# Kernel optimization log

Hardware: AMD Instinct MI355X
Metric: run time of the kernel (lower is better)

## Reference

```python
import jax, jax.numpy as jnp
import numpy as np

EPS = 1e-5


def _bn_relu(h, gamma, beta):
    # BatchNorm1d in training mode: stats over all but the last (channel) dim
    m = h.reshape(-1, h.shape[-1])
    mu = jnp.mean(m, axis=0)
    var = jnp.var(m, axis=0)
    return jax.nn.relu((h - mu) * jax.lax.rsqrt(var + EPS) * gamma + beta)


def setup_inputs() -> dict:
    key = jax.random.key(0)
    ks = jax.random.split(key, 16)
    B, N, D, OUT = 64, 64, 64, 128
    T = 2 * D          # object_tuple_size = 128
    HG, HF = 256, 128  # hidden_dim_g, hidden_dim_f

    def lin(k, i, o):
        return (jax.random.normal(k, (i, o), jnp.float32) / np.sqrt(i).astype(np.float32),
                jnp.zeros((o,), jnp.float32))

    inp = {"x": jax.random.normal(ks[0], (B, N, D), jnp.float32)}
    # G: depth-3 Linear-BN-ReLU, dims T -> HG -> HG -> T
    for i, (a, b) in enumerate([(T, HG), (HG, HG), (HG, T)]):
        W, bb = lin(ks[1 + i], a, b)
        inp[f"gW{i}"] = W
        inp[f"gb{i}"] = bb
        inp[f"gg{i}"] = jnp.ones((b,), jnp.float32)
        inp[f"gB{i}"] = jnp.zeros((b,), jnp.float32)
    # F: depth-2 Linear-BN-ReLU, dims T -> HF -> T, then Linear(T, OUT)
    for i, (a, b) in enumerate([(T, HF), (HF, T)]):
        W, bb = lin(ks[5 + i], a, b)
        inp[f"fW{i}"] = W
        inp[f"fb{i}"] = bb
        inp[f"fg{i}"] = jnp.ones((b,), jnp.float32)
        inp[f"fB{i}"] = jnp.zeros((b,), jnp.float32)
    inp["foW"], inp["fob"] = lin(ks[8], T, OUT)
    return inp


def reference(x, gW0, gb0, gg0, gB0, gW1, gb1, gg1, gB1, gW2, gb2, gg2, gB2,
              fW0, fb0, fg0, fB0, fW1, fb1, fg1, fB1, foW, fob):
    B, N, D = x.shape
    # GroupObjectsIntoPairs: all ordered pairs -> (B, N*N, 2D)
    xi = jnp.broadcast_to(x[:, :, None, :], (B, N, N, D))
    xj = jnp.broadcast_to(x[:, None, :, :], (B, N, N, D))
    h = jnp.concatenate([xi, xj], axis=-1).reshape(B, N * N, 2 * D)
    # G: per-pair MLP
    for W, b, g, be in ((gW0, gb0, gg0, gB0), (gW1, gb1, gg1, gB1), (gW2, gb2, gg2, gB2)):
        h = _bn_relu(h @ W + b, g, be)
    # sum over pair dimension (no layer norm)
    s = h.sum(axis=1)  # (B, 2D)
    # F: MLP + final linear
    for W, b, g, be in ((fW0, fb0, fg0, fB0), (fW1, fb1, fg1, fB1)):
        s = _bn_relu(s @ W + b, g, be)
    return s @ foW + fob  # (B, OUT)
```

## Files before the change

### kernel.cpp

```cpp
#include <hip/hip_runtime.h>


typedef _Float16 half8 __attribute__((ext_vector_type(8)));
typedef _Float16 half4_t __attribute__((ext_vector_type(4)));
typedef float float4_t __attribute__((ext_vector_type(4)));

static constexpr float kEps = 1e-5f;
static constexpr float kM = 262144.f;

static constexpr size_t OFF_U   = 0;
static constexpr size_t OFF_V   = OFF_U  + (size_t)4096*256*4;
static constexpr size_t OFF_UP  = OFF_V  + (size_t)4096*256*4;
static constexpr size_t OFF_VP  = OFF_UP + (size_t)4096*256*2;
static constexpr size_t OFF_W1T = OFF_VP + (size_t)4096*256*2;
static constexpr size_t OFF_W2T = OFF_W1T + (size_t)256*256*2;
static constexpr size_t OFF_Z1  = OFF_W2T + (size_t)128*256*2;
static constexpr size_t OFF_ST0 = OFF_Z1 + (size_t)262144*256*2;
static constexpr size_t OFF_C0S = OFF_ST0 + (size_t)64*4*256*4;
static constexpr size_t OFF_C0T = OFF_C0S + 1024;
static constexpr size_t OFF_C1S = OFF_C0T + 1024;
static constexpr size_t OFF_C1T = OFF_C1S + 1024;
static constexpr size_t OFF_C2S = OFF_C1T + 1024;
static constexpr size_t OFF_C2T = OFF_C2S + 512;
static constexpr size_t OFF_ST1 = OFF_C2T + 512;
static constexpr size_t OFF_ST2 = OFF_ST1 + (size_t)32*512*4;
static constexpr size_t OFF_SB  = OFF_ST2 + (size_t)32*256*4;
static constexpr size_t OFF_FST0 = OFF_SB + (size_t)64*128*4;
static constexpr size_t OFF_FST1 = OFF_FST0 + 1024;
static constexpr size_t ZERO_BYTES = (size_t)32*512*4 + (size_t)32*256*4
                                   + (size_t)64*128*4 + 2048;
static constexpr size_t OFF_FZ0  = OFF_FST1 + 1024;
static constexpr size_t OFF_FZ1  = OFF_FZ0 + (size_t)64*128*4;
static constexpr size_t OFF_CF0S = OFF_FZ1 + (size_t)64*128*4;
static constexpr size_t OFF_CF0T = OFF_CF0S + 512;
static constexpr size_t OFF_CF1S = OFF_CF0T + 512;
static constexpr size_t OFF_CF1T = OFF_CF1S + 512;
static constexpr size_t OFF_C1H  = OFF_CF1T + 512;
static constexpr size_t OFF_Z2   = OFF_C1H + 1024;
static constexpr size_t WS_REQUIRED = OFF_Z2 + (size_t)262144*128*2;

static __device__ inline half8 relu8(half8 s) {
#pragma unroll
  for (int e = 0; e < 8; ++e) s[e] = s[e] > (_Float16)0 ? s[e] : (_Float16)0;
  return s;
}

__global__ __launch_bounds__(256) void k_wt(const float* __restrict__ gW1,
                                            const float* __restrict__ gW2,
                                            _Float16* __restrict__ W1T,
                                            _Float16* __restrict__ W2T) {
  int idx = blockIdx.x * 256 + threadIdx.x;
  if (idx < 65536) {
    int n = idx >> 8, k = idx & 255;
    W1T[idx] = (_Float16)gW1[k * 256 + n];
  } else if (idx < 98304) {
    int j = idx - 65536;
    int n = j >> 8, k = j & 255;
    W2T[j] = (_Float16)gW2[k * 128 + n];
  }
}

__global__ __launch_bounds__(256) void k_prep(const float* __restrict__ x,
                                              const float* __restrict__ gW0,
                                              float* __restrict__ U,
                                              float* __restrict__ V) {
  __shared__ __align__(16) float sX[32 * 64];
  int t = threadIdx.x;
  int p0 = blockIdx.x * 32;
  int by = blockIdx.y;
  int hsel = by >> 1;
  int cbase = (by & 1) * 128;
#pragma unroll
  for (int it = 0; it < 2; ++it) {
    int f4 = (it * 256 + t) * 4;
    *(float4_t*)(sX + f4) = *(const float4_t*)(x + (size_t)p0 * 64 + f4);
  }
  __syncthreads();
  int r = t >> 3, cg = (t & 7) * 16;
  const float* Wb = gW0 + (size_t)(hsel * 64) * 256 + cbase + cg;
  float acc[16];
#pragma unroll
  for (int j = 0; j < 16; ++j) acc[j] = 0.f;
  for (int k = 0; k < 64; ++k) {
    float xv = sX[r * 64 + k];
    const float4_t* wr = (const float4_t*)(Wb + (size_t)k * 256);
    float4_t w0 = wr[0], w1 = wr[1], w2 = wr[2], w3 = wr[3];
#pragma unroll
    for (int j = 0; j < 4; ++j) {
      acc[j]      += xv * w0[j];
      acc[4 + j]  += xv * w1[j];
      acc[8 + j]  += xv * w2[j];
      acc[12 + j] += xv * w3[j];
    }
  }
  float* outp = (hsel ? V : U) + (size_t)(p0 + r) * 256 + cbase + cg;
#pragma unroll
  for (int q = 0; q < 4; ++q) {
    float4_t o = {acc[q * 4], acc[q * 4 + 1], acc[q * 4 + 2], acc[q * 4 + 3]};
    *(float4_t*)(outp + q * 4) = o;
  }
}

__global__ __launch_bounds__(256) void k_stats0(const float* __restrict__ U,
                                                const float* __restrict__ V,
                                                float* __restrict__ st0) {
  int b = blockIdx.x, c = threadIdx.x;
  float su = 0, su2 = 0, sv = 0, sv2 = 0;
  for (int i = 0; i < 64; ++i) {
    float u = U[(size_t)(b * 64 + i) * 256 + c];
    float v = V[(size_t)(b * 64 + i) * 256 + c];
    su += u; su2 += u * u; sv += v; sv2 += v * v;
  }
  st0[(b * 4 + 0) * 256 + c] = su;
  st0[(b * 4 + 1) * 256 + c] = su2;
  st0[(b * 4 + 2) * 256 + c] = sv;
  st0[(b * 4 + 3) * 256 + c] = sv2;
}

__global__ __launch_bounds__(256) void k_bn0(const float* __restrict__ st0,
                                             const float* __restrict__ gb0,
                                             const float* __restrict__ gg0,
                                             const float* __restrict__ gB0,
                                             float* __restrict__ c0s,
                                             float* __restrict__ c0t) {
  int c = threadIdx.x;
  float su = 0, su2 = 0, sv = 0, sv2 = 0, cross = 0;
  for (int b = 0; b < 64; ++b) {
    float a  = st0[(b * 4 + 0) * 256 + c];
    float a2 = st0[(b * 4 + 1) * 256 + c];
    float v  = st0[(b * 4 + 2) * 256 + c];
    float v2 = st0[(b * 4 + 3) * 256 + c];
    su += a; su2 += a2; sv += v; sv2 += v2; cross += a * v;
  }
  float b0 = gb0[c];
  float sumz  = 64.f * (su + sv) + kM * b0;
  float sumzz = 64.f * (su2 + sv2) + 2.f * cross + 2.f * b0 * 64.f * (su + sv) + kM * b0 * b0;
  float mu = sumz / kM;
  float var = sumzz / kM - mu * mu;
  float sc = gg0[c] * rsqrtf(var + kEps);
  c0s[c] = sc;
  c0t[c] = gB0[c] + sc * (b0 - mu);
}

__global__ __launch_bounds__(256) void k_uv(const float* __restrict__ U,
                                            const float* __restrict__ V,
                                            const float* __restrict__ c0s,
                                            const float* __restrict__ c0t,
                                            _Float16* __restrict__ Up,
                                            _Float16* __restrict__ Vp) {
  int idx = blockIdx.x * 256 + threadIdx.x;
  int e4 = idx * 4;
  int c4 = e4 & 255;
  float4_t u = *(const float4_t*)(U + e4);
  float4_t v = *(const float4_t*)(V + e4);
  float4_t s = *(const float4_t*)(c0s + c4);
  float4_t tt = *(const float4_t*)(c0t + c4);
  half4_t hu, hv;
#pragma unroll
  for (int e = 0; e < 4; ++e) {
    hu[e] = (_Float16)(u[e] * s[e] + tt[e]);
    hv[e] = (_Float16)(v[e] * s[e]);
  }
  *(half4_t*)(Up + e4) = hu;
  *(half4_t*)(Vp + e4) = hv;
}

__global__ __launch_bounds__(256) void k_gemm1(const _Float16* __restrict__ Up,
                                               const _Float16* __restrict__ Vp,
                                               const _Float16* __restrict__ W1T,
                                               const float* __restrict__ gb1,
                                               _Float16* __restrict__ Z1,
                                               float* __restrict__ stats1) {
  __shared__ __align__(16) char smem[128 * 136 * 2];
  _Float16* sU = (_Float16*)smem;
  _Float16* sV = (_Float16*)(smem + 288);
  _Float16* sW = (_Float16*)(smem + 288 + 64 * 72 * 2);
  _Float16* sO = (_Float16*)smem;

  const int t = threadIdx.x;
  const int bx = blockIdx.x;
  const int n0 = blockIdx.y * 128;
  const int b = bx >> 5;
  const int i0 = (bx & 31) * 2;
  const long R0 = (long)bx * 128;

  const int wid = t >> 6, L = t & 63;
  const int wrow = wid >> 1, wcol = wid & 1;
  const int quad = L >> 4, l15 = L & 15;

  float4_t acc[4][4];
#pragma unroll
  for (int mt = 0; mt < 4; ++mt)
#pragma unroll
    for (int nt = 0; nt < 4; ++nt) acc[mt][nt] = (float4_t){0.f, 0.f, 0.f, 0.f};

  for (int kc = 0; kc < 4; ++kc) {
    __syncthreads();
    if (t < 16) {
      int row = t >> 3, c8 = (t & 7) * 8;
      *(half8*)(sU + row * 72 + c8) =
          *(const half8*)(Up + (size_t)(b * 64 + i0 + row) * 256 + kc * 64 + c8);
    }
#pragma unroll
    for (int it = 0; it < 2; ++it) {
      int flat = it * 256 + t;
      int row = flat >> 3, c8 = (flat & 7) * 8;
      *(half8*)(sV + row * 72 + c8) =
          *(const half8*)(Vp + (size_t)(b * 64 + row) * 256 + kc * 64 + c8);
    }
#pragma unroll
    for (int it = 0; it < 4; ++it) {
      int flat = it * 256 + t;
      int row = flat >> 3, c8 = (flat & 7) * 8;
      *(half8*)(sW + row * 72 + c8) =
          *(const half8*)(W1T + (size_t)(n0 + row) * 256 + kc * 64 + c8);
    }
    __syncthreads();
#pragma unroll
    for (int ks = 0; ks < 2; ++ks) {
      const int kk = ks * 32 + quad * 8;
      const half8 u = *(const half8*)(sU + wrow * 72 + kk);
      half8 afr[4];
#pragma unroll
      for (int mt = 0; mt < 4; ++mt) {
        half8 v = *(const half8*)(sV + (mt * 16 + l15) * 72 + kk);
        afr[mt] = relu8(u + v);
      }
      half8 bfr[4];
#pragma unroll
      for (int nt = 0; nt < 4; ++nt)
        bfr[nt] = *(const half8*)(sW + (wcol * 64 + nt * 16 + l15) * 72 + kk);
#pragma unroll
      for (int mt = 0; mt < 4; ++mt)
#pragma unroll
        for (int nt = 0; nt < 4; ++nt)
          acc[mt][nt] = __builtin_amdgcn_mfma_f32_16x16x32_f16(afr[mt], bfr[nt],
                                                               acc[mt][nt], 0, 0, 0);
    }
  }

  __syncthreads();
  const int rep = bx & 31;
#pragma unroll
  for (int nt = 0; nt < 4; ++nt) {
    const int lcol = wcol * 64 + nt * 16 + l15;
    const float b1c = gb1[n0 + lcol];
    float sz = 0.f, szz = 0.f;
#pragma unroll
    for (int mt = 0; mt < 4; ++mt) {
      const int lrow = wrow * 64 + mt * 16 + quad * 4;
#pragma unroll
      for (int r = 0; r < 4; ++r) {
        float z = acc[mt][nt][r] + b1c;
        sO[(lrow + r) * 136 + lcol] = (_Float16)z;
        sz += z;
        szz += z * z;
      }
    }
    sz += __shfl_xor(sz, 16, 64);
    sz += __shfl_xor(sz, 32, 64);
    szz += __shfl_xor(szz, 16, 64);
    szz += __shfl_xor(szz, 32, 64);
    if (quad == 0) {
      atomicAdd(stats1 + rep * 512 + n0 + lcol, sz);
      atomicAdd(stats1 + rep * 512 + 256 + n0 + lcol, szz);
    }
  }
  __syncthreads();
#pragma unroll
  for (int it = 0; it < 8; ++it) {
    int cid = it * 256 + t;
    int row = cid >> 4, ch = (cid & 15) * 8;
    half8 hv = *(const half8*)(sO + row * 136 + ch);
    *(half8*)(Z1 + (size_t)(R0 + row) * 256 + n0 + ch) = hv;
  }
}

__global__ __launch_bounds__(256) void k_bn1(const float* __restrict__ stats1,
                                             const float* __restrict__ gg1,
                                             const float* __restrict__ gB1,
                                             float* __restrict__ c1s,
                                             float* __restrict__ c1t,
                                             _Float16* __restrict__ c1h) {
  int c = threadIdx.x;
  float S = 0.f, S2 = 0.f;
  for (int rp = 0; rp < 32; ++rp) {
    S += stats1[rp * 512 + c];
    S2 += stats1[rp * 512 + 256 + c];
  }
  float mu = S / kM;
  float var = S2 / kM - mu * mu;
  float sc = gg1[c] * rsqrtf(var + kEps);
  float sh = gB1[c] - sc * mu;
  c1s[c] = sc;
  c1t[c] = sh;
  c1h[c] = (_Float16)sc;
  c1h[256 + c] = (_Float16)sh;
}

__global__ __launch_bounds__(256) void k_gemm2(const _Float16* __restrict__ Z1,
                                               const _Float16* __restrict__ W2T,
                                               const _Float16* __restrict__ c1h,
                                               const float* __restrict__ gb2,
                                               _Float16* __restrict__ Z2,
                                               float* __restrict__ stats2) {
  __shared__ __align__(16) char smem[2 * 128 * 72 * 2];
  _Float16* sA = (_Float16*)smem;
  _Float16* sW = (_Float16*)(smem + 128 * 72 * 2);
  _Float16* sO = (_Float16*)smem;
  __shared__ __align__(16) _Float16 sSh[256];
  __shared__ __align__(16) _Float16 sTh[256];
  const int t = threadIdx.x;
  const int bx = blockIdx.x;
  const long R0 = (long)bx * 128;
  sSh[t] = c1h[t];
  sTh[t] = c1h[256 + t];

  const int wid = t >> 6, L = t & 63;
  const int wrow = wid >> 1, wcol = wid & 1;
  const int quad = L >> 4, l15 = L & 15;

  float4_t acc[4][4];
#pragma unroll
  for (int mt = 0; mt < 4; ++mt)
#pragma unroll
    for (int nt = 0; nt < 4; ++nt) acc[mt][nt] = (float4_t){0.f, 0.f, 0.f, 0.f};

  for (int kc = 0; kc < 4; ++kc) {
    __syncthreads();
#pragma unroll
    for (int it = 0; it < 2; ++it) {
      int flat = it * 256 + t;
      int row = flat >> 3, k8 = (flat & 7) * 8;
      int kg = kc * 64 + k8;
      half8 hv = *(const half8*)(Z1 + ((size_t)R0 + row) * 256 + kg);
      half8 hs = *(const half8*)(sSh + kg);
      half8 ht = *(const half8*)(sTh + kg);
      half8 ov = relu8(hv * hs + ht);
      *(half8*)(sA + row * 72 + k8) = ov;
      int row2 = row + 64;
      half8 hv2 = *(const half8*)(Z1 + ((size_t)R0 + row2) * 256 + kg);
      half8 ov2 = relu8(hv2 * hs + ht);
      *(half8*)(sA + row2 * 72 + k8) = ov2;
    }
#pragma unroll
    for (int it = 0; it < 4; ++it) {
      int flat = it * 256 + t;
      int row = flat >> 3, k8 = (flat & 7) * 8;
      *(half8*)(sW + row * 72 + k8) =
          *(const half8*)(W2T + (size_t)row * 256 + kc * 64 + k8);
    }
    __syncthreads();
#pragma unroll
    for (int ks = 0; ks < 2; ++ks) {
      const int kk = ks * 32 + quad * 8;
      half8 afr[4];
#pragma unroll
      for (int mt = 0; mt < 4; ++mt)
        afr[mt] = *(const half8*)(sA + (wrow * 64 + mt * 16 + l15) * 72 + kk);
      half8 bfr[4];
#pragma unroll
      for (int nt = 0; nt < 4; ++nt)
        bfr[nt] = *(const half8*)(sW + (wcol * 64 + nt * 16 + l15) * 72 + kk);
#pragma unroll
      for (int mt = 0; mt < 4; ++mt)
#pragma unroll
        for (int nt = 0; nt < 4; ++nt)
          acc[mt][nt] = __builtin_amdgcn_mfma_f32_16x16x32_f16(afr[mt], bfr[nt],
                                                               acc[mt][nt], 0, 0, 0);
    }
  }

  __syncthreads();
  const int rep = bx & 31;
#pragma unroll
  for (int nt = 0; nt < 4; ++nt) {
    const int lcol = wcol * 64 + nt * 16 + l15;
    const float b2c = gb2[lcol];
    float sz = 0.f, szz = 0.f;
#pragma unroll
    for (int mt = 0; mt < 4; ++mt) {
      const int lrow = wrow * 64 + mt * 16 + quad * 4;
#pragma unroll
      for (int r = 0; r < 4; ++r) {
        float z = acc[mt][nt][r] + b2c;
        sO[(lrow + r) * 136 + lcol] = (_Float16)z;
        sz += z;
        szz += z * z;
      }
    }
    sz += __shfl_xor(sz, 16, 64);
    sz += __shfl_xor(sz, 32, 64);
    szz += __shfl_xor(szz, 16, 64);
    szz += __shfl_xor(szz, 32, 64);
    if (quad == 0) {
      atomicAdd(stats2 + rep * 256 + lcol, sz);
      atomicAdd(stats2 + rep * 256 + 128 + lcol, szz);
    }
  }
  __syncthreads();
#pragma unroll
  for (int it = 0; it < 8; ++it) {
    int cid = it * 256 + t;
    int row = cid >> 4, ch = (cid & 15) * 8;
    half8 hv = *(const half8*)(sO + row * 136 + ch);
    *(half8*)(Z2 + (size_t)(R0 + row) * 128 + ch) = hv;
  }
}

template <int FINAL>
__global__ __launch_bounds__(256) void k_gemm23(const _Float16* __restrict__ Z1,
                                                const _Float16* __restrict__ W2T,
                                                const float* __restrict__ c1s,
                                                const float* __restrict__ c1t,
                                                const float* __restrict__ gb2,
                                                const float* __restrict__ c2s,
                                                const float* __restrict__ c2t,
                                                float* __restrict__ stats2,
                                                float* __restrict__ sbuf) {
  __shared__ __align__(16) _Float16 sA[128 * 72];
  __shared__ __align__(16) _Float16 sW[128 * 72];
  __shared__ __align__(16) float sS[256];
  __shared__ __align__(16) float sT[256];
  const int t = threadIdx.x;
  const int bx = blockIdx.x;
  const long R0 = (long)bx * 128;
  sS[t] = c1s[t];
  sT[t] = c1t[t];

  const int wid = t >> 6, L = t & 63;
  const int wrow = wid >> 1, wcol = wid & 1;
  const int quad = L >> 4, l15 = L & 15;

  float4_t acc[4][4];
#pragma unroll
  for (int mt = 0; mt < 4; ++mt)
#pragma unroll
    for (int nt = 0; nt < 4; ++nt) acc[mt][nt] = (float4_t){0.f, 0.f, 0.f, 0.f};

  for (int kc = 0; kc < 4; ++kc) {
    __syncthreads();
#pragma unroll
    for (int it = 0; it < 4; ++it) {
      int flat = it * 256 + t;
      int row = flat >> 3, k8 = (flat & 7) * 8;
      int kg = kc * 64 + k8;
      half8 hv = *(const half8*)(Z1 + ((size_t)R0 + row) * 256 + kg);
      float4_t s0 = *(const float4_t*)(sS + kg);
      float4_t s1 = *(const float4_t*)(sS + kg + 4);
      float4_t t0 = *(const float4_t*)(sT + kg);
      float4_t t1 = *(const float4_t*)(sT + kg + 4);
      half8 ov;
#pragma unroll
      for (int e = 0; e < 4; ++e) {
        ov[e]     = (_Float16)fmaxf(s0[e] * (float)hv[e] + t0[e], 0.f);
        ov[4 + e] = (_Float16)fmaxf(s1[e] * (float)hv[4 + e] + t1[e], 0.f);
      }
      *(half8*)(sA + row * 72 + k8) = ov;
    }
#pragma unroll
    for (int it = 0; it < 4; ++it) {
      int flat = it * 256 + t;
      int n = flat >> 3, k8 = (flat & 7) * 8;
      *(half8*)(sW + n * 72 + k8) =
          *(const half8*)(W2T + (size_t)n * 256 + kc * 64 + k8);
    }
    __syncthreads();
#pragma unroll
    for (int ks = 0; ks < 2; ++ks) {
      const int kk = ks * 32 + quad * 8;
      half8 afr[4];
#pragma unroll
      for (int mt = 0; mt < 4; ++mt)
        afr[mt] = *(const half8*)(sA + (wrow * 64 + mt * 16 + l15) * 72 + kk);
      half8 bfr[4];
#pragma unroll
      for (int nt = 0; nt < 4; ++nt)
        bfr[nt] = *(const half8*)(sW + (wcol * 64 + nt * 16 + l15) * 72 + kk);
#pragma unroll
      for (int mt = 0; mt < 4; ++mt)
#pragma unroll
        for (int nt = 0; nt < 4; ++nt)
          acc[mt][nt] = __builtin_amdgcn_mfma_f32_16x16x32_f16(afr[mt], bfr[nt],
                                                               acc[mt][nt], 0, 0, 0);
    }
  }

  const int rep = bx & 31;
#pragma unroll
  for (int nt = 0; nt < 4; ++nt) {
    const int col = wcol * 64 + nt * 16 + l15;
    const float b2c = gb2[col];
    if (FINAL) {
      const float s2 = c2s[col], t2 = c2t[col];
      float ps = 0.f;
#pragma unroll
      for (int mt = 0; mt < 4; ++mt)
#pragma unroll
        for (int r = 0; r < 4; ++r)
          ps += fmaxf(s2 * (acc[mt][nt][r] + b2c) + t2, 0.f);
      ps += __shfl_xor(ps, 16, 64);
      ps += __shfl_xor(ps, 32, 64);
      if (quad == 0) atomicAdd(sbuf + (bx >> 5) * 128 + col, ps);
    } else {
      float sz = 0.f, szz = 0.f;
#pragma unroll
      for (int mt = 0; mt < 4; ++mt)
#pragma unroll
        for (int r = 0; r < 4; ++r) {
          float z = acc[mt][nt][r] + b2c;
          sz += z;
          szz += z * z;
        }
      sz += __shfl_xor(sz, 16, 64);
      sz += __shfl_xor(sz, 32, 64);
      szz += __shfl_xor(szz, 16, 64);
      szz += __shfl_xor(szz, 32, 64);
      if (quad == 0) {
        atomicAdd(stats2 + rep * 256 + col, sz);
        atomicAdd(stats2 + rep * 256 + 128 + col, szz);
      }
    }
  }
}

__global__ __launch_bounds__(128) void k_bn2(const float* __restrict__ stats2,
                                             const float* __restrict__ gg2,
                                             const float* __restrict__ gB2,
                                             float* __restrict__ c2s,
                                             float* __restrict__ c2t) {
  int c = threadIdx.x;
  float S = 0.f, S2 = 0.f;
  for (int rp = 0; rp < 32; ++rp) {
    S += stats2[rp * 256 + c];
    S2 += stats2[rp * 256 + 128 + c];
  }
  float mu = S / kM;
  float var = S2 / kM - mu * mu;
  float sc = gg2[c] * rsqrtf(var + kEps);
  c2s[c] = sc;
  c2t[c] = gB2[c] - sc * mu;
}

__global__ __launch_bounds__(256) void k_red(const _Float16* __restrict__ Z2,
                                             const float* __restrict__ c2s,
                                             const float* __restrict__ c2t,
                                             float* __restrict__ sbuf) {
  __shared__ float sR[256 * 8];
  const int t = threadIdx.x;
  const int bx = blockIdx.x;
  const int b = bx >> 5;
  const long row0 = (long)bx * 128;
  const int rr = t >> 4;
  const int c8 = (t & 15) * 8;

  float4_t s0 = *(const float4_t*)(c2s + c8);
  float4_t s1 = *(const float4_t*)(c2s + c8 + 4);
  float4_t t0 = *(const float4_t*)(c2t + c8);
  float4_t t1 = *(const float4_t*)(c2t + c8 + 4);

  float acc[8];
#pragma unroll
  for (int e = 0; e < 8; ++e) acc[e] = 0.f;
#pragma unroll
  for (int it = 0; it < 8; ++it) {
    long row = row0 + it * 16 + rr;
    half8 h = *(const half8*)(Z2 + row * 128 + c8);
#pragma unroll
    for (int e = 0; e < 4; ++e) {
      acc[e]     += fmaxf(s0[e] * (float)h[e] + t0[e], 0.f);
      acc[4 + e] += fmaxf(s1[e] * (float)h[4 + e] + t1[e], 0.f);
    }
  }
#pragma unroll
  for (int e = 0; e < 8; ++e) sR[t * 8 + e] = acc[e];
  __syncthreads();
  if (t < 128) {
    float S = 0.f;
#pragma unroll
    for (int rr2 = 0; rr2 < 16; ++rr2) S += sR[rr2 * 128 + t];
    atomicAdd(sbuf + b * 128 + t, S);
  }
}

template <bool APPLY_BN, bool STATS>
__global__ __launch_bounds__(256) void k_fg(const float* __restrict__ in,
                                            const float* __restrict__ cs,
                                            const float* __restrict__ ct,
                                            const float* __restrict__ W,
                                            const float* __restrict__ bias,
                                            float* __restrict__ zout,
                                            float* __restrict__ stats) {
  __shared__ __align__(16) float sIn[8 * 128];
  __shared__ __align__(16) float sZ[8 * 128];
  const int t = threadIdx.x;
  const int r0 = blockIdx.x * 8;
  {
    int flat = t * 4;
    int col = flat & 127;
    float4_t v = *(const float4_t*)(in + (size_t)r0 * 128 + flat);
    if (APPLY_BN) {
      float4_t s = *(const float4_t*)(cs + col);
      float4_t sh = *(const float4_t*)(ct + col);
#pragma unroll
      for (int e = 0; e < 4; ++e) v[e] = fmaxf(s[e] * v[e] + sh[e], 0.f);
    }
    *(float4_t*)(sIn + flat) = v;
  }
  __syncthreads();

  const int r = t >> 5;
  const int c4 = (t & 31) * 4;
  float4_t acc = *(const float4_t*)(bias + c4);
  for (int k = 0; k < 128; ++k) {
    float xv = sIn[r * 128 + k];
    float4_t w = *(const float4_t*)(W + (size_t)k * 128 + c4);
#pragma unroll
    for (int e = 0; e < 4; ++e) acc[e] += xv * w[e];
  }
  *(float4_t*)(zout + (size_t)(r0 + r) * 128 + c4) = acc;

  if (STATS) {
    *(float4_t*)(sZ + r * 128 + c4) = acc;
    __syncthreads();
    if (t < 128) {
      float S = 0.f, S2 = 0.f;
#pragma unroll
      for (int rr = 0; rr < 8; ++rr) {
        float z = sZ[rr * 128 + t];
        S += z;
        S2 += z * z;
      }
      atomicAdd(stats + t, S);
      atomicAdd(stats + 128 + t, S2);
    }
  }
}

__global__ __launch_bounds__(128) void k_fbn(const float* __restrict__ stats,
                                             const float* __restrict__ g,
                                             const float* __restrict__ B,
                                             float* __restrict__ cs,
                                             float* __restrict__ ct) {
  int c = threadIdx.x;
  float S = stats[c], S2 = stats[128 + c];
  float mu = S / 64.f;
  float var = S2 / 64.f - mu * mu;
  float sc = g[c] * rsqrtf(var + kEps);
  cs[c] = sc;
  ct[c] = B[c] - sc * mu;
}

extern "C" void kernel_launch(void* const* d_in, const int* in_sizes, int n_in,
                              void* d_out, int out_size, void* d_ws, size_t ws_size,
                              hipStream_t stream) {
  (void)in_sizes; (void)n_in; (void)out_size;
  const float* x   = (const float*)d_in[0];
  const float* gW0 = (const float*)d_in[1];
  const float* gb0 = (const float*)d_in[2];
  const float* gg0 = (const float*)d_in[3];
  const float* gB0 = (const float*)d_in[4];
  const float* gW1 = (const float*)d_in[5];
  const float* gb1 = (const float*)d_in[6];
  const float* gg1 = (const float*)d_in[7];
  const float* gB1 = (const float*)d_in[8];
  const float* gW2 = (const float*)d_in[9];
  const float* gb2 = (const float*)d_in[10];
  const float* gg2 = (const float*)d_in[11];
  const float* gB2 = (const float*)d_in[12];
  const float* fW0 = (const float*)d_in[13];
  const float* fb0 = (const float*)d_in[14];
  const float* fg0 = (const float*)d_in[15];
  const float* fB0 = (const float*)d_in[16];
  const float* fW1 = (const float*)d_in[17];
  const float* fb1 = (const float*)d_in[18];
  const float* fg1 = (const float*)d_in[19];
  const float* fB1 = (const float*)d_in[20];
  const float* foW = (const float*)d_in[21];
  const float* fob = (const float*)d_in[22];
  float* out = (float*)d_out;

  char* ws = (char*)d_ws;
  float*    U    = (float*)(ws + OFF_U);
  float*    V    = (float*)(ws + OFF_V);
  _Float16* Up   = (_Float16*)(ws + OFF_UP);
  _Float16* Vp   = (_Float16*)(ws + OFF_VP);
  _Float16* W1T  = (_Float16*)(ws + OFF_W1T);
  _Float16* W2T  = (_Float16*)(ws + OFF_W2T);
  _Float16* Z1   = (_Float16*)(ws + OFF_Z1);
  float*    st0  = (float*)(ws + OFF_ST0);
  float*    c0s  = (float*)(ws + OFF_C0S);
  float*    c0t  = (float*)(ws + OFF_C0T);
  float*    c1s  = (float*)(ws + OFF_C1S);
  float*    c1t  = (float*)(ws + OFF_C1T);
  float*    c2s  = (float*)(ws + OFF_C2S);
  float*    c2t  = (float*)(ws + OFF_C2T);
  float*    st1  = (float*)(ws + OFF_ST1);
  float*    st2  = (float*)(ws + OFF_ST2);
  float*    sbuf = (float*)(ws + OFF_SB);
  float*    fst0 = (float*)(ws + OFF_FST0);
  float*    fst1 = (float*)(ws + OFF_FST1);
  float*    fz0  = (float*)(ws + OFF_FZ0);
  float*    fz1  = (float*)(ws + OFF_FZ1);
  float*    cf0s = (float*)(ws + OFF_CF0S);
  float*    cf0t = (float*)(ws + OFF_CF0T);
  float*    cf1s = (float*)(ws + OFF_CF1S);
  float*    cf1t = (float*)(ws + OFF_CF1T);
  _Float16* c1h  = (_Float16*)(ws + OFF_C1H);
  _Float16* Z2   = (_Float16*)(ws + OFF_Z2);

  hipMemsetAsync(ws + OFF_ST1, 0, ZERO_BYTES, stream);

  k_wt<<<384, 256, 0, stream>>>(gW1, gW2, W1T, W2T);
  k_prep<<<dim3(128, 4), 256, 0, stream>>>(x, gW0, U, V);
  k_stats0<<<64, 256, 0, stream>>>(U, V, st0);
  k_bn0<<<1, 256, 0, stream>>>(st0, gb0, gg0, gB0, c0s, c0t);
  k_uv<<<1024, 256, 0, stream>>>(U, V, c0s, c0t, Up, Vp);
  k_gemm1<<<dim3(2048, 2), 256, 0, stream>>>(Up, Vp, W1T, gb1, Z1, st1);
  k_bn1<<<1, 256, 0, stream>>>(st1, gg1, gB1, c1s, c1t, c1h);

  if (ws_size >= WS_REQUIRED) {
    k_gemm2<<<2048, 256, 0, stream>>>(Z1, W2T, c1h, gb2, Z2, st2);
    k_bn2<<<1, 128, 0, stream>>>(st2, gg2, gB2, c2s, c2t);
    k_red<<<2048, 256, 0, stream>>>(Z2, c2s, c2t, sbuf);
  } else {
    k_gemm23<0><<<2048, 256, 0, stream>>>(Z1, W2T, c1s, c1t, gb2, c2s, c2t, st2, sbuf);
    k_bn2<<<1, 128, 0, stream>>>(st2, gg2, gB2, c2s, c2t);
    k_gemm23<1><<<2048, 256, 0, stream>>>(Z1, W2T, c1s, c1t, gb2, c2s, c2t, st2, sbuf);
  }

  k_fg<false, true><<<8, 256, 0, stream>>>(sbuf, nullptr, nullptr, fW0, fb0, fz0, fst0);
  k_fbn<<<1, 128, 0, stream>>>(fst0, fg0, fB0, cf0s, cf0t);
  k_fg<true, true><<<8, 256, 0, stream>>>(fz0, cf0s, cf0t, fW1, fb1, fz1, fst1);
  k_fbn<<<1, 128, 0, stream>>>(fst1, fg1, fB1, cf1s, cf1t);
  k_fg<true, false><<<8, 256, 0, stream>>>(fz1, cf1s, cf1t, foW, fob, out, nullptr);
}
```

Measured before the change: 311.7 us.

## Restructure gemm1 to full-width N tile with 32x32 MFMA and precomputed A

The first pair GEMM now computes all 256 output columns per block with 512 threads, where before it split N across two grid blocks. The relu(u+v) A tile is formed once while loading shared memory instead of being recomputed per warp per fragment. The MFMA shape changes from 16x16x32 to 32x32x16, and the fp16 output goes out in two halves through shared memory. This is meant to remove the duplicate A construction and V reloads across the two N blocks and to cut LDS traffic, at the cost of more shared memory and registers per block.

```diff
diff --git a/kernel.cpp b/kernel.cpp
--- a/kernel.cpp
+++ b/kernel.cpp
@@ -4,6 +4,7 @@
 typedef _Float16 half8 __attribute__((ext_vector_type(8)));
 typedef _Float16 half4_t __attribute__((ext_vector_type(4)));
 typedef float float4_t __attribute__((ext_vector_type(4)));
+typedef float floatx16 __attribute__((ext_vector_type(16)));
 
 static constexpr float kEps = 1e-5f;
 static constexpr float kM = 262144.f;
@@ -165,114 +166,123 @@
   *(half4_t*)(Vp + e4) = hv;
 }
 
-__global__ __launch_bounds__(256) void k_gemm1(const _Float16* __restrict__ Up,
-                                               const _Float16* __restrict__ Vp,
-                                               const _Float16* __restrict__ W1T,
-                                               const float* __restrict__ gb1,
-                                               _Float16* __restrict__ Z1,
-                                               float* __restrict__ stats1) {
-  __shared__ __align__(16) char smem[128 * 136 * 2];
-  _Float16* sU = (_Float16*)smem;
-  _Float16* sV = (_Float16*)(smem + 288);
-  _Float16* sW = (_Float16*)(smem + 288 + 64 * 72 * 2);
+__global__ __launch_bounds__(512, 4) void k_gemm1(const _Float16* __restrict__ Up,
+                                                  const _Float16* __restrict__ Vp,
+                                                  const _Float16* __restrict__ W1T,
+                                                  const float* __restrict__ gb1,
+                                                  _Float16* __restrict__ Z1,
+                                                  float* __restrict__ stats1) {
+  __shared__ __align__(16) char smem[52224];
+  _Float16* sA = (_Float16*)smem;
+  _Float16* sW = (_Float16*)(smem + 17408);
   _Float16* sO = (_Float16*)smem;
 
   const int t = threadIdx.x;
   const int bx = blockIdx.x;
-  const int n0 = blockIdx.y * 128;
   const int b = bx >> 5;
   const int i0 = (bx & 31) * 2;
   const long R0 = (long)bx * 128;
 
   const int wid = t >> 6, L = t & 63;
-  const int wrow = wid >> 1, wcol = wid & 1;
-  const int quad = L >> 4, l15 = L & 15;
-
-  float4_t acc[4][4];
-#pragma unroll
-  for (int mt = 0; mt < 4; ++mt)
-#pragma unroll
-    for (int nt = 0; nt < 4; ++nt) acc[mt][nt] = (float4_t){0.f, 0.f, 0.f, 0.f};
+  const int wrow = wid >> 2, wcol = wid & 3;
+  const int l31 = L & 31, khalf = L >> 5;
+
+  const int arow = t >> 3;
+  const int ac8 = (t & 7) * 8;
+
+  floatx16 acc[2][2];
+#pragma unroll
+  for (int mt = 0; mt < 2; ++mt)
+#pragma unroll
+    for (int nt = 0; nt < 2; ++nt)
+#pragma unroll
+      for (int r = 0; r < 16; ++r) acc[mt][nt][r] = 0.f;
 
   for (int kc = 0; kc < 4; ++kc) {
     __syncthreads();
-    if (t < 16) {
-      int row = t >> 3, c8 = (t & 7) * 8;
-      *(half8*)(sU + row * 72 + c8) =
-          *(const half8*)(Up + (size_t)(b * 64 + i0 + row) * 256 + kc * 64 + c8);
-    }
-#pragma unroll
-    for (int it = 0; it < 2; ++it) {
-      int flat = it * 256 + t;
+    {
+      const int kg = kc * 64 + ac8;
+      half8 u0 = *(const half8*)(Up + (size_t)(b * 64 + i0) * 256 + kg);
+      half8 u1 = *(const half8*)(Up + (size_t)(b * 64 + i0 + 1) * 256 + kg);
+      half8 v  = *(const half8*)(Vp + (size_t)(b * 64 + arow) * 256 + kg);
+      *(half8*)(sA + arow * 68 + ac8) = relu8(u0 + v);
+      *(half8*)(sA + (64 + arow) * 68 + ac8) = relu8(u1 + v);
+    }
+#pragma unroll
+    for (int it = 0; it < 4; ++it) {
+      int flat = it * 512 + t;
       int row = flat >> 3, c8 = (flat & 7) * 8;
-      *(half8*)(sV + row * 72 + c8) =
-          *(const half8*)(Vp + (size_t)(b * 64 + row) * 256 + kc * 64 + c8);
-    }
-#pragma unroll
-    for (int it = 0; it < 4; ++it) {
-      int flat = it * 256 + t;
-      int row = flat >> 3, c8 = (flat & 7) * 8;
-      *(half8*)(sW + row * 72 + c8) =
-          *(const half8*)(W1T + (size_t)(n0 + row) * 256 + kc * 64 + c8);
-    }
-    __syncthreads();
-#pragma unroll
-    for (int ks = 0; ks < 2; ++ks) {
-      const int kk = ks * 32 + quad * 8;
-      const half8 u = *(const half8*)(sU + wrow * 72 + kk);
-      half8 afr[4];
-#pragma unroll
-      for (int mt = 0; mt < 4; ++mt) {
-        half8 v = *(const half8*)(sV + (mt * 16 + l15) * 72 + kk);
-        afr[mt] = relu8(u + v);
-      }
-      half8 bfr[4];
-#pragma unroll
-      for (int nt = 0; nt < 4; ++nt)
-        bfr[nt] = *(const half8*)(sW + (wcol * 64 + nt * 16 + l15) * 72 + kk);
-#pragma unroll
-      for (int mt = 0; mt < 4; ++mt)
-#pragma unroll
-        for (int nt = 0; nt < 4; ++nt)
-          acc[mt][nt] = __builtin_amdgcn_mfma_f32_16x16x32_f16(afr[mt], bfr[nt],
+      *(half8*)(sW + row * 68 + c8) =
+          *(const half8*)(W1T + (size_t)row * 256 + kc * 64 + c8);
+    }
+    __syncthreads();
+#pragma unroll
+    for (int ks = 0; ks < 4; ++ks) {
+      const int kk = ks * 16 + khalf * 8;
+      half8 afr[2], bfr[2];
+#pragma unroll
+      for (int mt = 0; mt < 2; ++mt)
+        afr[mt] = *(const half8*)(sA + (wrow * 64 + mt * 32 + l31) * 68 + kk);
+#pragma unroll
+      for (int nt = 0; nt < 2; ++nt)
+        bfr[nt] = *(const half8*)(sW + (wcol * 64 + nt * 32 + l31) * 68 + kk);
+#pragma unroll
+      for (int mt = 0; mt < 2; ++mt)
+#pragma unroll
+        for (int nt = 0; nt < 2; ++nt)
+          acc[mt][nt] = __builtin_amdgcn_mfma_f32_32x32x16_f16(afr[mt], bfr[nt],
                                                                acc[mt][nt], 0, 0, 0);
     }
   }
 
-  __syncthreads();
   const int rep = bx & 31;
 #pragma unroll
-  for (int nt = 0; nt < 4; ++nt) {
-    const int lcol = wcol * 64 + nt * 16 + l15;
-    const float b1c = gb1[n0 + lcol];
+  for (int nt = 0; nt < 2; ++nt) {
+    const int col = wcol * 64 + nt * 32 + l31;
+    const float b1c = gb1[col];
     float sz = 0.f, szz = 0.f;
 #pragma unroll
-    for (int mt = 0; mt < 4; ++mt) {
-      const int lrow = wrow * 64 + mt * 16 + quad * 4;
-#pragma unroll
-      for (int r = 0; r < 4; ++r) {
+    for (int mt = 0; mt < 2; ++mt)
+#pragma unroll
+      for (int r = 0; r < 16; ++r) {
         float z = acc[mt][nt][r] + b1c;
-        sO[(lrow + r) * 136 + lcol] = (_Float16)z;
+        acc[mt][nt][r] = z;
         sz += z;
         szz += z * z;
       }
-    }
-    sz += __shfl_xor(sz, 16, 64);
     sz += __shfl_xor(sz, 32, 64);
-    szz += __shfl_xor(szz, 16, 64);
     szz += __shfl_xor(szz, 32, 64);
-    if (quad == 0) {
-      atomicAdd(stats1 + rep * 512 + n0 + lcol, sz);
-      atomicAdd(stats1 + rep * 512 + 256 + n0 + lcol, szz);
-    }
-  }
-  __syncthreads();
-#pragma unroll
-  for (int it = 0; it < 8; ++it) {
-    int cid = it * 256 + t;
-    int row = cid >> 4, ch = (cid & 15) * 8;
-    half8 hv = *(const half8*)(sO + row * 136 + ch);
-    *(half8*)(Z1 + (size_t)(R0 + row) * 256 + n0 + ch) = hv;
+    if (L < 32) {
+      atomicAdd(stats1 + rep * 512 + col, sz);
+      atomicAdd(stats1 + rep * 512 + 256 + col, szz);
+    }
+  }
+
+#pragma unroll
+  for (int p = 0; p < 2; ++p) {
+    __syncthreads();
+    if ((wcol >> 1) == p) {
+      const int colh = (wcol & 1) * 64;
+#pragma unroll
+      for (int nt = 0; nt < 2; ++nt) {
+        const int lc = colh + nt * 32 + l31;
+#pragma unroll
+        for (int mt = 0; mt < 2; ++mt)
+#pragma unroll
+          for (int r = 0; r < 16; ++r) {
+            int rowf = (r & 3) + 8 * (r >> 2) + 4 * khalf;
+            sO[(wrow * 64 + mt * 32 + rowf) * 136 + lc] = (_Float16)acc[mt][nt][r];
+          }
+      }
+    }
+    __syncthreads();
+#pragma unroll
+    for (int it = 0; it < 4; ++it) {
+      int cid = it * 512 + t;
+      int row = cid >> 4, ch = (cid & 15) * 8;
+      half8 hv = *(const half8*)(sO + row * 136 + ch);
+      *(half8*)(Z1 + (size_t)(R0 + row) * 256 + p * 128 + ch) = hv;
+    }
   }
 }
 
@@ -716,7 +726,7 @@
   k_stats0<<<64, 256, 0, stream>>>(U, V, st0);
   k_bn0<<<1, 256, 0, stream>>>(st0, gb0, gg0, gB0, c0s, c0t);
   k_uv<<<1024, 256, 0, stream>>>(U, V, c0s, c0t, Up, Vp);
-  k_gemm1<<<dim3(2048, 2), 256, 0, stream>>>(Up, Vp, W1T, gb1, Z1, st1);
+  k_gemm1<<<2048, 512, 0, stream>>>(Up, Vp, W1T, gb1, Z1, st1);
   k_bn1<<<1, 256, 0, stream>>>(st1, gg1, gB1, c1s, c1t, c1h);
 
   if (ws_size >= WS_REQUIRED) {
```

Measured after the change: 386.0 us. 1.24x slower.
